# Kernel optimization log

Measured on AMD Instinct MI355X. Metric: run time of the kernel, lower is better.

## Reference

```python
import jax, jax.numpy as jnp
import numpy as np

B, S, H, NH = 8, 1024, 1024, 16
HD = H // NH  # head dim = 64

def setup_inputs() -> dict:
    key = jax.random.key(0)
    ks = jax.random.split(key, 7)
    sc = 0.02
    return {
        "activation": jax.random.normal(ks[0], (B, S, H), jnp.float32),
        "qw": jax.random.normal(ks[1], (H, H), jnp.float32) * sc,
        "qb": jax.random.normal(ks[2], (H,), jnp.float32) * sc,
        "kw": jax.random.normal(ks[3], (H, H), jnp.float32) * sc,
        "kb": jax.random.normal(ks[4], (H,), jnp.float32) * sc,
        "vw": jax.random.normal(ks[5], (H, H), jnp.float32) * sc,
        "vb": jax.random.normal(ks[6], (H,), jnp.float32) * sc,
    }

def reference(activation, qw, qb, kw, kb, vw, vb):
    # QKV projections (torch Linear: x @ W^T + b)
    def proj(x, w, b):
        y = jnp.einsum('bsh,oh->bso', x, w) + b
        # split heads: [B,S,H] -> [B,NH,S,HD]
        return y.reshape(B, S, NH, HD).transpose(0, 2, 1, 3)
    q = proj(activation, qw, qb)
    k = proj(activation, kw, kb)
    v = proj(activation, vw, vb)
    # NOTE: source scales by 1/sqrt(hidden_dim), NOT 1/sqrt(head_dim)
    scale = 1.0 / jnp.sqrt(jnp.float32(H))
    scores = jnp.einsum('bnqd,bnkd->bnqk', q, k) * scale
    probs = jax.nn.softmax(scores, axis=-1)
    ctx = jnp.einsum('bnqk,bnkd->bnqd', probs, v)
    # merge heads: [B,NH,S,HD] -> [B,S,H]
    return ctx.transpose(0, 2, 1, 3).reshape(B, S, H)
```

## Files before the change

### kernel.cpp

```cpp
#include <hip/hip_runtime.h>
#include <cstdint>
#include <cstddef>

#define B_   8
#define S_   1024
#define H_   1024
#define NH_  16
#define HD_  64
#define M_   8192
#define N3_  3072
#define K_   1024

typedef __attribute__((ext_vector_type(8))) short bf16x8;
typedef __attribute__((ext_vector_type(4))) float f32x4;
typedef __attribute__((ext_vector_type(16))) float f32x16;
typedef __attribute__((ext_vector_type(8))) unsigned short u16x8;
typedef __attribute__((ext_vector_type(4))) unsigned u32x4;

__device__ __forceinline__ unsigned short f2bf(float f) {
  unsigned u = __builtin_bit_cast(unsigned, f);
  u += 0x7fffu + ((u >> 16) & 1u);
  return (unsigned short)(u >> 16);
}

__device__ __forceinline__ unsigned cvtpk(float a, float b) {
  unsigned r;
  asm("v_cvt_pk_bf16_f32 %0, %1, %2" : "=v"(r) : "v"(a), "v"(b));
  return r;
}

__global__ void cvt_kernel(const float* __restrict__ src,
                           unsigned short* __restrict__ dst, int n) {
  const int stride = gridDim.x * blockDim.x * 8;
  for (int i = (blockIdx.x * blockDim.x + threadIdx.x) * 8; i < n; i += stride) {
    float4 a = *reinterpret_cast<const float4*>(src + i);
    float4 b = *reinterpret_cast<const float4*>(src + i + 4);
    u16x8 o;
    o[0] = f2bf(a.x); o[1] = f2bf(a.y); o[2] = f2bf(a.z); o[3] = f2bf(a.w);
    o[4] = f2bf(b.x); o[5] = f2bf(b.y); o[6] = f2bf(b.z); o[7] = f2bf(b.w);
    *reinterpret_cast<u16x8*>(dst + i) = o;
  }
}

__global__ void wcvt_kernel(const float* __restrict__ q,
                            const float* __restrict__ k,
                            const float* __restrict__ v,
                            unsigned short* __restrict__ dst) {
  const int i = (blockIdx.x * blockDim.x + threadIdx.x) * 8;
  const float* src;
  int off;
  if (i < 1048576)      { src = q; off = i; }
  else if (i < 2097152) { src = k; off = i - 1048576; }
  else                  { src = v; off = i - 2097152; }
  float4 a = *reinterpret_cast<const float4*>(src + off);
  float4 b = *reinterpret_cast<const float4*>(src + off + 4);
  u16x8 o;
  o[0] = f2bf(a.x); o[1] = f2bf(a.y); o[2] = f2bf(a.z); o[3] = f2bf(a.w);
  o[4] = f2bf(b.x); o[5] = f2bf(b.y); o[6] = f2bf(b.z); o[7] = f2bf(b.w);
  *reinterpret_cast<u16x8*>(dst + i) = o;
}

__global__ __launch_bounds__(512, 4) void qkv_gemm(
    const unsigned short* __restrict__ A,
    const unsigned short* __restrict__ Bw,
    const float* __restrict__ qb, const float* __restrict__ kb,
    const float* __restrict__ vb,
    unsigned short* __restrict__ Qh,
    unsigned short* __restrict__ Kh,
    unsigned short* __restrict__ Vth)
{
  extern __shared__ char sm[];
  const int t = threadIdx.x;
  const int lane = t & 63;
  const int wave = t >> 6;
  const int wm = wave >> 1;
  const int wn = wave & 1;

  const int bid = blockIdx.x;
  const int chunk = bid >> 3;
  const int bm = (bid & 7) * 4 + chunk / 24;
  const int bn = chunk % 24;

  const char* Ab = (const char*)A + (size_t)bm * 256 * 2048;
  const char* Bb = (const char*)Bw + (size_t)bn * 128 * 2048;

  f32x4 acc[4][4] = {};

  #define STG3(kt, buf)                                                        \
    { char* Ad = sm + (buf) * 24576;                                           \
      _Pragma("unroll")                                                        \
      for (int j = 0; j < 2; ++j) {                                            \
        const int off = j * 8192 + t * 16;                                     \
        const int r = off >> 6;                                                \
        const int sc = ((off >> 4) & 3) ^ ((r >> 1) & 3);                      \
        __builtin_amdgcn_global_load_lds(                                      \
          (const __attribute__((address_space(1))) void*)(Ab + r * 2048 + (kt) * 64 + sc * 16), \
          (__attribute__((address_space(3))) void*)(Ad + off), 16, 0, 0);      \
      }                                                                        \
      { const int off = t * 16;                                                \
        const int r = off >> 6;                                                \
        const int sc = ((off >> 4) & 3) ^ ((r >> 1) & 3);                      \
        __builtin_amdgcn_global_load_lds(                                      \
          (const __attribute__((address_space(1))) void*)(Bb + r * 2048 + (kt) * 64 + sc * 16), \
          (__attribute__((address_space(3))) void*)(Ad + 16384 + off), 16, 0, 0); } }

  STG3(0, 0)
  STG3(1, 1)
  asm volatile("s_waitcnt vmcnt(3)" ::: "memory");
  __builtin_amdgcn_s_barrier();

  for (int kt = 0; kt < 32; ++kt) {
    const char* Abuf = sm + (kt % 3) * 24576;
    const char* Bbuf = Abuf + 16384;
    bf16x8 afr[4], bfr[4];
    #pragma unroll
    for (int f = 0; f < 4; ++f) {
      const int r = wm * 64 + f * 16 + (lane & 15);
      afr[f] = *(const bf16x8*)(Abuf + r * 64 + (((lane >> 4) ^ ((r >> 1) & 3)) << 4));
    }
    #pragma unroll
    for (int g = 0; g < 4; ++g) {
      const int r = wn * 64 + g * 16 + (lane & 15);
      bfr[g] = *(const bf16x8*)(Bbuf + r * 64 + (((lane >> 4) ^ ((r >> 1) & 3)) << 4));
    }
    if (kt < 30) STG3(kt + 2, (kt + 2) % 3)
    __builtin_amdgcn_s_setprio(1);
    #pragma unroll
    for (int f = 0; f < 4; ++f)
      #pragma unroll
      for (int g = 0; g < 4; ++g)
        acc[f][g] = __builtin_amdgcn_mfma_f32_16x16x32_bf16(
            afr[f], bfr[g], acc[f][g], 0, 0, 0);
    __builtin_amdgcn_s_setprio(0);
    if (kt < 30)       asm volatile("s_waitcnt vmcnt(3)" ::: "memory");
    else if (kt == 30) asm volatile("s_waitcnt vmcnt(0)" ::: "memory");
    if (kt < 31) __builtin_amdgcn_s_barrier();
  }

  const int tensor = bn >> 3;
  const float* bias = (tensor == 0) ? qb : (tensor == 1) ? kb : vb;
  const float scl = (tensor == 0) ? 0.04508422f : 1.0f;
  #pragma unroll
  for (int g = 0; g < 4; ++g) {
    const int col = bn * 128 + wn * 64 + g * 16 + (lane & 15);
    const int o  = col & 1023;
    const int nhh = o >> 6, hd = o & 63;
    const float bv = bias[o];
    #pragma unroll
    for (int f = 0; f < 4; ++f) {
      #pragma unroll
      for (int r = 0; r < 4; ++r) {
        const int i = bm * 256 + wm * 64 + f * 16 + (lane >> 4) * 4 + r;
        const int bb = i >> 10, s = i & 1023;
        const unsigned short hval = f2bf((acc[f][g][r] + bv) * scl);
        const int bhn = bb * NH_ + nhh;
        if (tensor == 0)      Qh[((size_t)bhn * S_ + s) * HD_ + hd] = hval;
        else if (tensor == 1) Kh[((size_t)bhn * S_ + s) * HD_ + hd] = hval;
        else                  Vth[(size_t)bhn * 65536 + (s >> 6) * 4096 + hd * 64 + (s & 63)] = hval;
      }
    }
  }
}

__device__ __forceinline__ bf16x8 mk_frag(const f32x16& s, const int base) {
  unsigned a0 = cvtpk(s[base + 0], s[base + 1]);
  unsigned a1 = cvtpk(s[base + 2], s[base + 3]);
  unsigned b0 = cvtpk(s[base + 4], s[base + 5]);
  unsigned b1 = cvtpk(s[base + 6], s[base + 7]);
  asm("v_permlane32_swap_b32 %0, %1" : "+v"(a0), "+v"(b0));
  asm("v_permlane32_swap_b32 %0, %1" : "+v"(a1), "+v"(b1));
  u32x4 u = {a0, a1, b0, b1};
  return __builtin_bit_cast(bf16x8, u);
}

__global__ __launch_bounds__(256, 3) void attn_kernel(
    const unsigned short* __restrict__ Qh,
    const unsigned short* __restrict__ Kh,
    const unsigned short* __restrict__ Vth,
    float* __restrict__ Out)
{
  __shared__ char smx[2][16384];
  const int t = threadIdx.x;
  const int lane = t & 63;
  const int wave = t >> 6;
  const int l31 = lane & 31;
  const int hi = lane >> 5;
  const int hw = blockIdx.x;
  const int xcd = hw & 7;
  const int qt = (hw >> 3) & 7;
  const int bh = (hw >> 6) * 8 + xcd;
  const int b = bh >> 4, nh = bh & 15;

  const unsigned short* Qp = Qh + (size_t)bh * (S_ * HD_);
  const char* Kp = (const char*)Kh + (size_t)bh * 131072;
  const char* Vp = (const char*)Vth + (size_t)bh * 131072;
  const int q0 = qt * 128 + wave * 32;

  bf16x8 bq[4];
  #pragma unroll
  for (int st = 0; st < 4; ++st)
    bq[st] = *reinterpret_cast<const bf16x8*>(
        Qp + (size_t)(q0 + l31) * HD_ + st * 16 + hi * 8);

  const int soff0 = wave * 1024 + lane * 16;
  #define STAGE_TILE(dstbase, srcbase)                                            \
    _Pragma("unroll")                                                             \
    for (int j = 0; j < 2; ++j) {                                                 \
      const int off = j * 4096 + soff0;                                           \
      const int row = off >> 7;                                                   \
      const int sc  = ((off >> 4) & 7) ^ (row & 7);                               \
      __builtin_amdgcn_global_load_lds(                                           \
          (const __attribute__((address_space(1))) void*)((srcbase) + row * 128 + sc * 16), \
          (__attribute__((address_space(3))) void*)((dstbase) + off), 16, 0, 0);  \
    }

  STAGE_TILE(&smx[0][0],    Kp)
  STAGE_TILE(&smx[0][8192], Vp)
  __syncthreads();

  f32x16 o0 = {}, o1 = {};
  float lsum = 0.f;
  const int swr = l31 & 7;

  for (int kt = 0; kt < 16; ++kt) {
    const int cur = kt & 1;
    if (kt < 15) {
      STAGE_TILE(&smx[cur ^ 1][0],    Kp + (kt + 1) * 8192)
      STAGE_TILE(&smx[cur ^ 1][8192], Vp + (kt + 1) * 8192)
    }
    const char* Kb = &smx[cur][0];
    const char* Vb = &smx[cur][8192];

    f32x16 s0 = {}, s1 = {};
    #pragma unroll
    for (int st = 0; st < 4; ++st) {
      const int c = ((st * 2 + hi) ^ swr) << 4;
      bf16x8 ka = *reinterpret_cast<const bf16x8*>(Kb + l31 * 128 + c);
      bf16x8 kc = *reinterpret_cast<const bf16x8*>(Kb + (l31 + 32) * 128 + c);
      s0 = __builtin_amdgcn_mfma_f32_32x32x16_bf16(ka, bq[st], s0, 0, 0, 0);
      s1 = __builtin_amdgcn_mfma_f32_32x32x16_bf16(kc, bq[st], s1, 0, 0, 0);
    }

    bf16x8 va[4];
    #pragma unroll
    for (int ks = 0; ks < 2; ++ks) {
      const int c = ((ks * 2 + hi) ^ swr) << 4;
      va[ks * 2]     = *reinterpret_cast<const bf16x8*>(Vb + l31 * 128 + c);
      va[ks * 2 + 1] = *reinterpret_cast<const bf16x8*>(Vb + (l31 + 32) * 128 + c);
    }
    #pragma unroll
    for (int r = 0; r < 16; ++r) {
      s0[r] = __builtin_amdgcn_exp2f(s0[r]);
      lsum += s0[r];
    }
    bf16x8 f0 = mk_frag(s0, 0);
    bf16x8 f1 = mk_frag(s0, 8);
    o0 = __builtin_amdgcn_mfma_f32_32x32x16_bf16(f0, va[0], o0, 0, 0, 0);
    o1 = __builtin_amdgcn_mfma_f32_32x32x16_bf16(f0, va[1], o1, 0, 0, 0);
    o0 = __builtin_amdgcn_mfma_f32_32x32x16_bf16(f1, va[2], o0, 0, 0, 0);
    o1 = __builtin_amdgcn_mfma_f32_32x32x16_bf16(f1, va[3], o1, 0, 0, 0);

    #pragma unroll
    for (int ks = 0; ks < 2; ++ks) {
      const int c = (((ks + 2) * 2 + hi) ^ swr) << 4;
      va[ks * 2]     = *reinterpret_cast<const bf16x8*>(Vb + l31 * 128 + c);
      va[ks * 2 + 1] = *reinterpret_cast<const bf16x8*>(Vb + (l31 + 32) * 128 + c);
    }
    #pragma unroll
    for (int r = 0; r < 16; ++r) {
      s1[r] = __builtin_amdgcn_exp2f(s1[r]);
      lsum += s1[r];
    }
    bf16x8 f2 = mk_frag(s1, 0);
    bf16x8 f3 = mk_frag(s1, 8);
    o0 = __builtin_amdgcn_mfma_f32_32x32x16_bf16(f2, va[0], o0, 0, 0, 0);
    o1 = __builtin_amdgcn_mfma_f32_32x32x16_bf16(f2, va[1], o1, 0, 0, 0);
    o0 = __builtin_amdgcn_mfma_f32_32x32x16_bf16(f3, va[2], o0, 0, 0, 0);
    o1 = __builtin_amdgcn_mfma_f32_32x32x16_bf16(f3, va[3], o1, 0, 0, 0);

    __syncthreads();
  }

  const float ltot = lsum + __shfl_xor(lsum, 32);
  const float inv = 1.0f / ltot;
  #pragma unroll
  for (int r = 0; r < 16; ++r) {
    const int crow = (r & 3) + 8 * (r >> 2) + 4 * hi;
    const float invq = __shfl(inv, crow);
    float* op = Out + ((size_t)(b * S_ + q0 + crow)) * H_ + nh * HD_ + l31;
    op[0]  = o0[r] * invq;
    op[32] = o1[r] * invq;
  }
}

extern "C" void kernel_launch(void* const* d_in, const int* in_sizes, int n_in,
                              void* d_out, int out_size, void* d_ws, size_t ws_size,
                              hipStream_t stream) {
  const float* act = (const float*)d_in[0];
  const float* qw  = (const float*)d_in[1];
  const float* qb  = (const float*)d_in[2];
  const float* kw  = (const float*)d_in[3];
  const float* kb  = (const float*)d_in[4];
  const float* vw  = (const float*)d_in[5];
  const float* vb  = (const float*)d_in[6];

  char* ws = (char*)d_ws;
  unsigned short* actb = (unsigned short*)ws;
  unsigned short* wb   = (unsigned short*)(ws + 16777216);
  unsigned short* Qh   = (unsigned short*)(ws + 23068672);
  unsigned short* Kh   = Qh + 8388608;
  unsigned short* Vth  = Kh + 8388608;

  cvt_kernel<<<4096, 256, 0, stream>>>(act, actb, M_ * K_);
  wcvt_kernel<<<1536, 256, 0, stream>>>(qw, kw, vw, wb);

  hipFuncSetAttribute((const void*)qkv_gemm,
                      hipFuncAttributeMaxDynamicSharedMemorySize, 73728);
  qkv_gemm<<<768, 512, 73728, stream>>>(actb, wb, qb, kb, vb, Qh, Kh, Vth);

  attn_kernel<<<1024, 256, 0, stream>>>(Qh, Kh, Vth, (float*)d_out);
}
```

Baseline: 146.4 us.

## Retile QKV GEMM to 128x128 blocks with K=64 stages and LDS-staged epilogue

The QKV projection GEMM moves from 512-thread 256x128 tiles with a triple-buffered K=32 pipeline to 256-thread 128x128 tiles with a double-buffered K=64 pipeline and a new XOR swizzle. The epilogue now stages bias-added bf16 results through shared memory and writes Q/K/V-transposed outputs as 16-byte vector stores, replacing the scattered 2-byte global stores. The aim is to cut uncoalesced write traffic and sync overhead. In exchange, smaller M tiles mean more reloading of the activation operand, and the shallower pipeline may hide less latency.

```diff
diff --git a/kernel.cpp b/kernel.cpp
--- a/kernel.cpp
+++ b/kernel.cpp
@@ -21,6 +21,14 @@
   unsigned u = __builtin_bit_cast(unsigned, f);
   u += 0x7fffu + ((u >> 16) & 1u);
   return (unsigned short)(u >> 16);
+}
+
+__device__ __forceinline__ unsigned long long pack4bf(float a, float b,
+                                                      float c, float d) {
+  return (unsigned long long)f2bf(a)
+       | ((unsigned long long)f2bf(b) << 16)
+       | ((unsigned long long)f2bf(c) << 32)
+       | ((unsigned long long)f2bf(d) << 48);
 }
 
 __device__ __forceinline__ unsigned cvtpk(float a, float b) {
@@ -60,7 +68,7 @@
   *reinterpret_cast<u16x8*>(dst + i) = o;
 }
 
-__global__ __launch_bounds__(512, 4) void qkv_gemm(
+__global__ __launch_bounds__(256, 2) void qkv_gemm(
     const unsigned short* __restrict__ A,
     const unsigned short* __restrict__ Bw,
     const float* __restrict__ qb, const float* __restrict__ kb,
@@ -72,92 +80,130 @@
   extern __shared__ char sm[];
   const int t = threadIdx.x;
   const int lane = t & 63;
-  const int wave = t >> 6;
-  const int wm = wave >> 1;
-  const int wn = wave & 1;
+  const int wm = t >> 7, wn = (t >> 6) & 1;
 
   const int bid = blockIdx.x;
-  const int chunk = bid >> 3;
-  const int bm = (bid & 7) * 4 + chunk / 24;
-  const int bn = chunk % 24;
-
-  const char* Ab = (const char*)A + (size_t)bm * 256 * 2048;
+  const int c = bid >> 3;
+  const int bm = (bid & 7) * 8 + c / 24;
+  const int bn = c % 24;
+
+  const char* Ab = (const char*)A + (size_t)bm * 128 * 2048;
   const char* Bb = (const char*)Bw + (size_t)bn * 128 * 2048;
 
   f32x4 acc[4][4] = {};
 
-  #define STG3(kt, buf)                                                        \
-    { char* Ad = sm + (buf) * 24576;                                           \
+  #define STG(kt, buf)                                                         \
+    { char* Ld = sm + (buf) * 32768;                                           \
       _Pragma("unroll")                                                        \
-      for (int j = 0; j < 2; ++j) {                                            \
-        const int off = j * 8192 + t * 16;                                     \
-        const int r = off >> 6;                                                \
-        const int sc = ((off >> 4) & 3) ^ ((r >> 1) & 3);                      \
+      for (int i = 0; i < 4; ++i) {                                            \
+        const int off = (i * 256 + t) * 16;                                    \
+        const int row = off >> 7;                                              \
+        const int sc  = ((off >> 4) & 7) ^ (row & 7);                          \
         __builtin_amdgcn_global_load_lds(                                      \
-          (const __attribute__((address_space(1))) void*)(Ab + r * 2048 + (kt) * 64 + sc * 16), \
-          (__attribute__((address_space(3))) void*)(Ad + off), 16, 0, 0);      \
-      }                                                                        \
-      { const int off = t * 16;                                                \
-        const int r = off >> 6;                                                \
-        const int sc = ((off >> 4) & 3) ^ ((r >> 1) & 3);                      \
+          (const __attribute__((address_space(1))) void*)(Ab + (size_t)row * 2048 + (kt) * 128 + sc * 16), \
+          (__attribute__((address_space(3))) void*)(Ld + off), 16, 0, 0);      \
         __builtin_amdgcn_global_load_lds(                                      \
-          (const __attribute__((address_space(1))) void*)(Bb + r * 2048 + (kt) * 64 + sc * 16), \
-          (__attribute__((address_space(3))) void*)(Ad + 16384 + off), 16, 0, 0); } }
-
-  STG3(0, 0)
-  STG3(1, 1)
-  asm volatile("s_waitcnt vmcnt(3)" ::: "memory");
-  __builtin_amdgcn_s_barrier();
-
-  for (int kt = 0; kt < 32; ++kt) {
-    const char* Abuf = sm + (kt % 3) * 24576;
-    const char* Bbuf = Abuf + 16384;
-    bf16x8 afr[4], bfr[4];
-    #pragma unroll
-    for (int f = 0; f < 4; ++f) {
-      const int r = wm * 64 + f * 16 + (lane & 15);
-      afr[f] = *(const bf16x8*)(Abuf + r * 64 + (((lane >> 4) ^ ((r >> 1) & 3)) << 4));
-    }
-    #pragma unroll
-    for (int g = 0; g < 4; ++g) {
-      const int r = wn * 64 + g * 16 + (lane & 15);
-      bfr[g] = *(const bf16x8*)(Bbuf + r * 64 + (((lane >> 4) ^ ((r >> 1) & 3)) << 4));
-    }
-    if (kt < 30) STG3(kt + 2, (kt + 2) % 3)
-    __builtin_amdgcn_s_setprio(1);
-    #pragma unroll
-    for (int f = 0; f < 4; ++f)
-      #pragma unroll
-      for (int g = 0; g < 4; ++g)
-        acc[f][g] = __builtin_amdgcn_mfma_f32_16x16x32_bf16(
-            afr[f], bfr[g], acc[f][g], 0, 0, 0);
-    __builtin_amdgcn_s_setprio(0);
-    if (kt < 30)       asm volatile("s_waitcnt vmcnt(3)" ::: "memory");
-    else if (kt == 30) asm volatile("s_waitcnt vmcnt(0)" ::: "memory");
-    if (kt < 31) __builtin_amdgcn_s_barrier();
+          (const __attribute__((address_space(1))) void*)(Bb + (size_t)row * 2048 + (kt) * 128 + sc * 16), \
+          (__attribute__((address_space(3))) void*)(Ld + 16384 + off), 16, 0, 0); \
+      } }
+
+  STG(0, 0)
+  __syncthreads();
+
+  for (int kt = 0; kt < 16; ++kt) {
+    if (kt < 15) STG(kt + 1, (kt + 1) & 1)
+    const char* Acur = sm + (kt & 1) * 32768;
+    const char* Bcur = Acur + 16384;
+    #pragma unroll
+    for (int kk = 0; kk < 2; ++kk) {
+      bf16x8 af[4], bf[4];
+      #pragma unroll
+      for (int mb = 0; mb < 4; ++mb) {
+        const int row = wm * 64 + mb * 16 + (lane & 15);
+        const int j   = kk * 4 + (lane >> 4);
+        af[mb] = *(const bf16x8*)(Acur + row * 128 + ((j ^ (row & 7)) << 4));
+      }
+      #pragma unroll
+      for (int nb = 0; nb < 4; ++nb) {
+        const int row = wn * 64 + nb * 16 + (lane & 15);
+        const int j   = kk * 4 + (lane >> 4);
+        bf[nb] = *(const bf16x8*)(Bcur + row * 128 + ((j ^ (row & 7)) << 4));
+      }
+      __builtin_amdgcn_s_setprio(1);
+      #pragma unroll
+      for (int mb = 0; mb < 4; ++mb)
+        #pragma unroll
+        for (int nb = 0; nb < 4; ++nb)
+          acc[mb][nb] = __builtin_amdgcn_mfma_f32_16x16x32_bf16(
+              af[mb], bf[nb], acc[mb][nb], 0, 0, 0);
+      __builtin_amdgcn_s_setprio(0);
+    }
+    __syncthreads();
   }
 
   const int tensor = bn >> 3;
+  const float scl = (tensor == 0) ? 0.04508422f : 1.0f;
   const float* bias = (tensor == 0) ? qb : (tensor == 1) ? kb : vb;
-  const float scl = (tensor == 0) ? 0.04508422f : 1.0f;
-  #pragma unroll
-  for (int g = 0; g < 4; ++g) {
-    const int col = bn * 128 + wn * 64 + g * 16 + (lane & 15);
-    const int o  = col & 1023;
-    const int nhh = o >> 6, hd = o & 63;
-    const float bv = bias[o];
-    #pragma unroll
-    for (int f = 0; f < 4; ++f) {
-      #pragma unroll
-      for (int r = 0; r < 4; ++r) {
-        const int i = bm * 256 + wm * 64 + f * 16 + (lane >> 4) * 4 + r;
-        const int bb = i >> 10, s = i & 1023;
-        const unsigned short hval = f2bf((acc[f][g][r] + bv) * scl);
-        const int bhn = bb * NH_ + nhh;
-        if (tensor == 0)      Qh[((size_t)bhn * S_ + s) * HD_ + hd] = hval;
-        else if (tensor == 1) Kh[((size_t)bhn * S_ + s) * HD_ + hd] = hval;
-        else                  Vth[(size_t)bhn * 65536 + (s >> 6) * 4096 + hd * 64 + (s & 63)] = hval;
+  char* E = sm;
+  const int bloc = bm >> 3;
+  const int srow = (bm & 7) * 128;
+
+  if (tensor < 2) {
+    #pragma unroll
+    for (int nb = 0; nb < 4; ++nb) {
+      const int col = wn * 64 + nb * 16 + (lane & 15);
+      const float bv = bias[(bn & 7) * 128 + col];
+      #pragma unroll
+      for (int mb = 0; mb < 4; ++mb) {
+        #pragma unroll
+        for (int r = 0; r < 4; ++r) {
+          const int row = wm * 64 + mb * 16 + (lane >> 4) * 4 + r;
+          const int byo = row * 256 + ((((col >> 3) ^ (row & 7)) << 4) | ((col & 7) << 1));
+          *(unsigned short*)(E + byo) = f2bf((acc[mb][nb][r] + bv) * scl);
+        }
       }
+    }
+    __syncthreads();
+    unsigned short* dst = (tensor == 0) ? Qh : Kh;
+    #pragma unroll
+    for (int cch = 0; cch < 8; ++cch) {
+      const int o = t * 128 + cch * 16;
+      const int row = o >> 8;
+      const int colb = o & 255;
+      const int col = colb >> 1;
+      u32x4 v = *(const u32x4*)(E + row * 256 + ((((colb >> 4) ^ (row & 7)) << 4)));
+      const int sg = srow + row;
+      const int nhh = (bn & 7) * 2 + (col >> 6);
+      const size_t db = ((size_t)(bloc * NH_ + nhh) * S_ + sg) * 128 + (col & 63) * 2;
+      *(u32x4*)((char*)dst + db) = v;
+    }
+  } else {
+    #pragma unroll
+    for (int nb = 0; nb < 4; ++nb) {
+      const int col = wn * 64 + nb * 16 + (lane & 15);
+      const float bv = bias[(bn & 7) * 128 + col];
+      #pragma unroll
+      for (int mb = 0; mb < 4; ++mb) {
+        const int row0 = wm * 64 + mb * 16 + (lane >> 4) * 4;
+        unsigned long long w = pack4bf(acc[mb][nb][0] + bv, acc[mb][nb][1] + bv,
+                                       acc[mb][nb][2] + bv, acc[mb][nb][3] + bv);
+        const int byo = col * 256 + ((((row0 >> 3) ^ (col & 7)) << 4) | ((row0 & 7) << 1));
+        *(unsigned long long*)(E + byo) = w;
+      }
+    }
+    __syncthreads();
+    #pragma unroll
+    for (int cch = 0; cch < 8; ++cch) {
+      const int o = t * 128 + cch * 16;
+      const int col = o >> 8;
+      const int rowb = o & 255;
+      const int row0 = rowb >> 1;
+      u32x4 v = *(const u32x4*)(E + col * 256 + ((((rowb >> 4) ^ (col & 7)) << 4)));
+      const int sg0 = srow + row0;
+      const int nhh = (bn & 7) * 2 + (col >> 6);
+      const size_t db = (size_t)(bloc * NH_ + nhh) * 131072 +
+                        (size_t)(sg0 >> 6) * 8192 + (col & 63) * 128 + (sg0 & 63) * 2;
+      *(u32x4*)((char*)Vth + db) = v;
     }
   }
 }
@@ -315,8 +361,8 @@
   wcvt_kernel<<<1536, 256, 0, stream>>>(qw, kw, vw, wb);
 
   hipFuncSetAttribute((const void*)qkv_gemm,
-                      hipFuncAttributeMaxDynamicSharedMemorySize, 73728);
-  qkv_gemm<<<768, 512, 73728, stream>>>(actb, wb, qb, kb, vb, Qh, Kh, Vth);
+                      hipFuncAttributeMaxDynamicSharedMemorySize, 65536);
+  qkv_gemm<<<1536, 256, 65536, stream>>>(actb, wb, qb, kb, vb, Qh, Kh, Vth);
 
   attn_kernel<<<1024, 256, 0, stream>>>(Qh, Kh, Vth, (float*)d_out);
 }
```

After: 123.5 us. -15.7%, faster.
